# Performance work log

Hardware: AMD Instinct MI355X
Metric: run time of the kernel (lower is better)

The kernel has to match this reference:

```python
import jax, jax.numpy as jnp
import numpy as np

# state_composition -> (modality, length); slices are consecutive offsets into D_state
COMP = [("joint_pos", 64), ("joint_vel", 64), ("eef_pose", 32), ("force", 32)]
NUM_EMB = 32   # num_embodiments
HID = 512      # hidden_size
EMB = 1024     # embed_dim
B, T = 16, 32


def setup_inputs() -> dict:
    key = jax.random.key(0)
    ks = iter(jax.random.split(key, 64))
    D = sum(L for _, L in COMP)
    inp = {
        "state_btD": jax.random.normal(next(ks), (B, T, D), jnp.float32),
        "embodiment_id_bt1": jax.random.randint(next(ks), (B, T, 1), 0, NUM_EMB, dtype=jnp.int64),
    }
    for m, L in COMP:
        inp[f"W1_{m}"] = 0.02 * jax.random.normal(next(ks), (NUM_EMB, L, HID), jnp.float32)
        inp[f"b1_{m}"] = jnp.zeros((NUM_EMB, HID), jnp.float32)
        inp[f"W2_{m}"] = 0.02 * jax.random.normal(next(ks), (NUM_EMB, HID, EMB), jnp.float32)
        inp[f"b2_{m}"] = jnp.zeros((NUM_EMB, EMB), jnp.float32)
        inp[f"te_{m}"] = 0.02 * jax.random.normal(next(ks), (1, 1, EMB), jnp.float32)
    return inp


def _cat_mlp(x, cat, W1, b1, W2, b2):
    # x: (N, in_dim), cat: (N,) int ids. Mirrors CategorySpecificMLP:
    # per-token weight gather W[cat] then bmm (here einsum over the token axis).
    h = jax.nn.relu(jnp.einsum("ni,nih->nh", x, W1[cat]) + b1[cat])
    return jnp.einsum("nh,nhe->ne", h, W2[cat]) + b2[cat]


def reference(state_btD, embodiment_id_bt1,
              W1_joint_pos, b1_joint_pos, W2_joint_pos, b2_joint_pos, te_joint_pos,
              W1_joint_vel, b1_joint_vel, W2_joint_vel, b2_joint_vel, te_joint_vel,
              W1_eef_pose, b1_eef_pose, W2_eef_pose, b2_eef_pose, te_eef_pose,
              W1_force, b1_force, W2_force, b2_force, te_force):
    Bv, Tv, D = state_btD.shape
    # expand (B,1,1) -> (B,T,1) if needed, then flatten to per-token ids
    cat = jnp.broadcast_to(embodiment_id_bt1, (Bv, Tv, 1)).reshape(Bv * Tv)
    params = [
        (W1_joint_pos, b1_joint_pos, W2_joint_pos, b2_joint_pos, te_joint_pos),
        (W1_joint_vel, b1_joint_vel, W2_joint_vel, b2_joint_vel, te_joint_vel),
        (W1_eef_pose, b1_eef_pose, W2_eef_pose, b2_eef_pose, te_eef_pose),
        (W1_force, b1_force, W2_force, b2_force, te_force),
    ]
    toks = []
    off = 0
    for (m, L), (W1, b1, W2, b2, te) in zip(COMP, params):
        x = state_btD[..., off:off + L].reshape(Bv * Tv, L)
        off += L
        z = _cat_mlp(x, cat, W1, b1, W2, b2) + te.reshape(EMB)
        toks.append(z.reshape(Bv, Tv, 1, EMB))
    return jnp.concatenate(toks, axis=2)  # (B, T, M, embed_dim)
```

## Files before the change

### kernel.cpp

```cpp
#include <hip/hip_runtime.h>

#define NCAT 32
#define NTOK 512
#define HID  512
#define EMB  1024
#define DSTATE 192
#define CHUNK 32
#define MAXW 48


__global__ __launch_bounds__(512) void bucket_kernel(
    const int* __restrict__ ids, int* __restrict__ cnt, int* __restrict__ nW,
    int* __restrict__ work, int* __restrict__ toklist)
{
    __shared__ int scnt[NCAT];
    const int tid = threadIdx.x;
    if (tid < NCAT) scnt[tid] = 0;
    __syncthreads();
    const int c = ids[tid];
    const int pos = atomicAdd(&scnt[c], 1);
    toklist[c * NTOK + pos] = tid;
    __syncthreads();
    if (tid == 0) {
        int n1 = 0;
        for (int cc = 0; cc < NCAT; ++cc) {
            const int n = scnt[cc];
            cnt[cc] = n;
            for (int ch = 0; ch * CHUNK < n; ++ch) work[n1++] = cc | (ch << 8);
        }
        nW[0] = n1;
    }
}

__device__ __forceinline__ void async_copy16(void* lds_dst, const void* g_src) {
    __builtin_amdgcn_global_load_lds(
        (__attribute__((address_space(1))) void*)(g_src),
        (__attribute__((address_space(3))) void*)(lds_dst),
        16, 0, 0);
}

__global__ __launch_bounds__(256, 2) void layer1_kernel(
    const float* __restrict__ state,
    const int* __restrict__ cnt, const int* __restrict__ toklist,
    const int* __restrict__ nW, const int* __restrict__ work,
    const float* __restrict__ W1_0, const float* __restrict__ W1_1,
    const float* __restrict__ W1_2, const float* __restrict__ W1_3,
    const float* __restrict__ b1_0, const float* __restrict__ b1_1,
    const float* __restrict__ b1_2, const float* __restrict__ b1_3,
    float* __restrict__ H)
{
    const int slot = blockIdx.x, mod = blockIdx.y, z = blockIdx.z;
    if (slot >= nW[0]) return;
    const int ent = work[slot];
    const int cat = ent & 255, chunk = ent >> 8;
    const int nC = cnt[cat];
    const int start = chunk * CHUNK;
    int nThis = nC - start;
    if (nThis > CHUNK) nThis = CHUNK;
    const int tid = threadIdx.x;
    const int tg = tid >> 6;
    const int cg = tid & 63;

    const int L   = (mod < 2) ? 64 : 32;
    const int off = (mod == 0) ? 0 : (mod == 1) ? 64 : (mod == 2) ? 128 : 160;

    __shared__ float sX[64 * 32];
    __shared__ int sTok[CHUNK];
    if (tid < CHUNK) sTok[tid] = (tid < nThis) ? toklist[cat * NTOK + start + tid] : 0;
    __syncthreads();

    {
        const int tt = tid & 31, kg = tid >> 5;
        const int rpk = L >> 3;
        const float* src = state + (size_t)sTok[tt] * DSTATE + off + kg * rpk;
        const bool ok = tt < nThis;
        for (int j = 0; j < (rpk >> 2); ++j) {
            float4 v = make_float4(0.f, 0.f, 0.f, 0.f);
            if (ok) v = ((const float4*)src)[j];
            const int k0 = kg * rpk + (j << 2);
            sX[(k0 + 0) * 32 + tt] = v.x;
            sX[(k0 + 1) * 32 + tt] = v.y;
            sX[(k0 + 2) * 32 + tt] = v.z;
            sX[(k0 + 3) * 32 + tt] = v.w;
        }
    }
    __syncthreads();

    const float* W1 = (mod == 0) ? W1_0 : (mod == 1) ? W1_1 : (mod == 2) ? W1_2 : W1_3;
    const float* b1 = (mod == 0) ? b1_0 : (mod == 1) ? b1_1 : (mod == 2) ? b1_2 : b1_3;
    const int colA = z * 256 + (cg << 2);
    const float* Wc = W1 + (size_t)cat * L * HID + colA;
    const int hbase = tg << 3;
    const bool act = hbase < nThis;

    float4 acc[8];
#pragma unroll
    for (int i = 0; i < 8; ++i) acc[i] = make_float4(0.f, 0.f, 0.f, 0.f);

    if (act) {
#pragma unroll 4
        for (int k = 0; k < L; ++k) {
            const float4 w  = *(const float4*)(Wc + (size_t)k * HID);
            const float4 h0 = *(const float4*)(sX + k * 32 + hbase);
            const float4 h1 = *(const float4*)(sX + k * 32 + hbase + 4);
#define L1FMA(i, s) acc[i].x += (s)*w.x; acc[i].y += (s)*w.y; \
                    acc[i].z += (s)*w.z; acc[i].w += (s)*w.w;
            L1FMA(0, h0.x) L1FMA(1, h0.y) L1FMA(2, h0.z) L1FMA(3, h0.w)
            L1FMA(4, h1.x) L1FMA(5, h1.y) L1FMA(6, h1.z) L1FMA(7, h1.w)
#undef L1FMA
        }
    }

    const float4 b = *(const float4*)(b1 + cat * HID + colA);
#pragma unroll
    for (int i = 0; i < 8; ++i) {
        const int t = hbase + i;
        if (t >= nThis) break;
        float4 h;
        h.x = acc[i].x + b.x; h.x = h.x > 0.f ? h.x : 0.f;
        h.y = acc[i].y + b.y; h.y = h.y > 0.f ? h.y : 0.f;
        h.z = acc[i].z + b.z; h.z = h.z > 0.f ? h.z : 0.f;
        h.w = acc[i].w + b.w; h.w = h.w > 0.f ? h.w : 0.f;
        *(float4*)(H + (size_t)(sTok[t] * 4 + mod) * HID + colA) = h;
    }
}

__global__ __launch_bounds__(256, 1) void layer2_kernel(
    const int* __restrict__ cnt, const int* __restrict__ toklist,
    const int* __restrict__ nW, const int* __restrict__ work,
    const float* __restrict__ H,
    const float* __restrict__ W2_0, const float* __restrict__ W2_1,
    const float* __restrict__ W2_2, const float* __restrict__ W2_3,
    const float* __restrict__ b2_0, const float* __restrict__ b2_1,
    const float* __restrict__ b2_2, const float* __restrict__ b2_3,
    const float* __restrict__ te_0, const float* __restrict__ te_1,
    const float* __restrict__ te_2, const float* __restrict__ te_3,
    float* __restrict__ out)
{
    const int slot = blockIdx.x, mod = blockIdx.y, z = blockIdx.z;
    if (slot >= nW[0]) return;
    const int ent = work[slot];
    const int cat = ent & 255, chunk = ent >> 8;
    const int nC = cnt[cat];
    const int start = chunk * CHUNK;
    int nThis = nC - start;
    if (nThis > CHUNK) nThis = CHUNK;
    const int tid = threadIdx.x;
    const int tg = tid >> 6;
    const int cg = tid & 63;
    const int zbase = z * 512;

    __shared__ float sH[512 * 32];
    __shared__ float wbuf[2][8 * 512];
    __shared__ int sTok[CHUNK];

    if (tid < CHUNK) sTok[tid] = (tid < nThis) ? toklist[cat * NTOK + start + tid] : 0;
    __syncthreads();

    const float* W2 = (mod == 0) ? W2_0 : (mod == 1) ? W2_1 : (mod == 2) ? W2_2 : W2_3;
    const float* Wc = W2 + (size_t)cat * (HID * EMB) + zbase;

#define STAGE_TILE(T, wb) do {                                                  \
        const float* gsrc_ = Wc + (size_t)((T) * 8 + (tid >> 7)) * EMB          \
                             + ((tid & 127) << 2);                              \
        float* ldst_ = (wb) + ((tid >> 6) << 8);                                \
        async_copy16(ldst_,        gsrc_);                                      \
        async_copy16(ldst_ + 1024, gsrc_ + 2 * EMB);                            \
        async_copy16(ldst_ + 2048, gsrc_ + 4 * EMB);                            \
        async_copy16(ldst_ + 3072, gsrc_ + 6 * EMB);                            \
    } while (0)

    STAGE_TILE(0, wbuf[0]);

    {
        const int tt = tid & 31, kg = tid >> 5;
        const float* src = H + (size_t)(sTok[tt] * 4 + mod) * HID + (kg << 6);
        const bool ok = tt < nThis;
#pragma unroll
        for (int j = 0; j < 16; ++j) {
            float4 v = make_float4(0.f, 0.f, 0.f, 0.f);
            if (ok) v = ((const float4*)src)[j];
            const int k0 = (kg << 6) + (j << 2);
            sH[(k0 + 0) * 32 + tt] = v.x;
            sH[(k0 + 1) * 32 + tt] = v.y;
            sH[(k0 + 2) * 32 + tt] = v.z;
            sH[(k0 + 3) * 32 + tt] = v.w;
        }
    }
    __syncthreads();

    const int hbase = tg << 3;
    const int wcol  = cg << 2;
    const bool act  = hbase < nThis;

    float4 a0[8], a1[8];
#pragma unroll
    for (int i = 0; i < 8; ++i) {
        a0[i] = make_float4(0.f, 0.f, 0.f, 0.f);
        a1[i] = make_float4(0.f, 0.f, 0.f, 0.f);
    }

#pragma unroll 1
    for (int T = 0; T < 64; ++T) {
        if (T + 1 < 64) STAGE_TILE(T + 1, wbuf[(T + 1) & 1]);
        if (act) {
            const float* wb = wbuf[T & 1];
            const int kb = T << 3;
#pragma unroll
            for (int r = 0; r < 8; ++r) {
                const float4 h0 = *(const float4*)(sH + (kb + r) * 32 + hbase);
                const float4 h1 = *(const float4*)(sH + (kb + r) * 32 + hbase + 4);
                const float4 w0 = *(const float4*)(wb + r * 512 + wcol);
                const float4 w1 = *(const float4*)(wb + r * 512 + 256 + wcol);
#define FMA2(i, s) a0[i].x += (s)*w0.x; a0[i].y += (s)*w0.y;                    \
                   a0[i].z += (s)*w0.z; a0[i].w += (s)*w0.w;                    \
                   a1[i].x += (s)*w1.x; a1[i].y += (s)*w1.y;                    \
                   a1[i].z += (s)*w1.z; a1[i].w += (s)*w1.w;
                FMA2(0, h0.x) FMA2(1, h0.y) FMA2(2, h0.z) FMA2(3, h0.w)
                FMA2(4, h1.x) FMA2(5, h1.y) FMA2(6, h1.z) FMA2(7, h1.w)
#undef FMA2
            }
        }
        __syncthreads();
    }
#undef STAGE_TILE

    const float* b2 = (mod == 0) ? b2_0 : (mod == 1) ? b2_1 : (mod == 2) ? b2_2 : b2_3;
    const float* te = (mod == 0) ? te_0 : (mod == 1) ? te_1 : (mod == 2) ? te_2 : te_3;
    const int colA = zbase + wcol;
    const int colB = colA + 256;
    const float4 bA = *(const float4*)(b2 + cat * EMB + colA);
    const float4 bB = *(const float4*)(b2 + cat * EMB + colB);
    const float4 tA = *(const float4*)(te + colA);
    const float4 tB = *(const float4*)(te + colB);
#pragma unroll
    for (int i = 0; i < 8; ++i) {
        const int t = hbase + i;
        if (t >= nThis) break;
        float* op = out + (size_t)(sTok[t] * 4 + mod) * EMB;
        *(float4*)(op + colA) = make_float4(a0[i].x + bA.x + tA.x,
                                            a0[i].y + bA.y + tA.y,
                                            a0[i].z + bA.z + tA.z,
                                            a0[i].w + bA.w + tA.w);
        *(float4*)(op + colB) = make_float4(a1[i].x + bB.x + tB.x,
                                            a1[i].y + bB.y + tB.y,
                                            a1[i].z + bB.z + tB.z,
                                            a1[i].w + bB.w + tB.w);
    }
}

extern "C" void kernel_launch(void* const* d_in, const int* in_sizes, int n_in,
                              void* d_out, int out_size, void* d_ws, size_t ws_size,
                              hipStream_t stream) {
    const float* state = (const float*)d_in[0];
    const int*   ids   = (const int*)d_in[1];
    const float *W1[4], *b1[4], *W2[4], *b2[4], *te[4];
    for (int m = 0; m < 4; ++m) {
        W1[m] = (const float*)d_in[2 + 5 * m + 0];
        b1[m] = (const float*)d_in[2 + 5 * m + 1];
        W2[m] = (const float*)d_in[2 + 5 * m + 2];
        b2[m] = (const float*)d_in[2 + 5 * m + 3];
        te[m] = (const float*)d_in[2 + 5 * m + 4];
    }
    char* ws = (char*)d_ws;
    int*   cnt     = (int*)ws;
    int*   nW      = (int*)(ws + 128);
    int*   work    = (int*)(ws + 256);
    int*   toklist = (int*)(ws + 1024);
    float* H       = (float*)(ws + 66560);
    float* out     = (float*)d_out;

    bucket_kernel<<<1, 512, 0, stream>>>(ids, cnt, nW, work, toklist);
    layer1_kernel<<<dim3(MAXW, 4, 2), 256, 0, stream>>>(
        state, cnt, toklist, nW, work,
        W1[0], W1[1], W1[2], W1[3],
        b1[0], b1[1], b1[2], b1[3], H);
    layer2_kernel<<<dim3(MAXW, 4, 2), 256, 0, stream>>>(
        cnt, toklist, nW, work, H,
        W2[0], W2[1], W2[2], W2[3],
        b2[0], b2[1], b2[2], b2[3],
        te[0], te[1], te[2], te[3], out);
}
```

Before: 340.6 us.

## Fuse layer1 into layer2 kernel with swizzled LDS hidden tile and triple-buffered W2

Merges the two MLP layer kernels into one. Each block computes the full 512-wide hidden activation for its 32-token chunk straight into a swizzled shared-memory tile, so the global H round trip and one kernel launch go away. The W2 staging pipeline moves from double to triple buffering with explicit vmcnt waits and raw barriers to keep more loads in flight. In exchange, layer1 work is repeated across the two z-halves, and LDS use grows, which may limit occupancy.

```diff
diff --git a/kernel.cpp b/kernel.cpp
--- a/kernel.cpp
+++ b/kernel.cpp
@@ -39,7 +39,7 @@
         16, 0, 0);
 }
 
-__global__ __launch_bounds__(256, 2) void layer1_kernel(
+__global__ __launch_bounds__(256, 1) void fused_kernel(
     const float* __restrict__ state,
     const int* __restrict__ cnt, const int* __restrict__ toklist,
     const int* __restrict__ nW, const int* __restrict__ work,
@@ -47,88 +47,6 @@
     const float* __restrict__ W1_2, const float* __restrict__ W1_3,
     const float* __restrict__ b1_0, const float* __restrict__ b1_1,
     const float* __restrict__ b1_2, const float* __restrict__ b1_3,
-    float* __restrict__ H)
-{
-    const int slot = blockIdx.x, mod = blockIdx.y, z = blockIdx.z;
-    if (slot >= nW[0]) return;
-    const int ent = work[slot];
-    const int cat = ent & 255, chunk = ent >> 8;
-    const int nC = cnt[cat];
-    const int start = chunk * CHUNK;
-    int nThis = nC - start;
-    if (nThis > CHUNK) nThis = CHUNK;
-    const int tid = threadIdx.x;
-    const int tg = tid >> 6;
-    const int cg = tid & 63;
-
-    const int L   = (mod < 2) ? 64 : 32;
-    const int off = (mod == 0) ? 0 : (mod == 1) ? 64 : (mod == 2) ? 128 : 160;
-
-    __shared__ float sX[64 * 32];
-    __shared__ int sTok[CHUNK];
-    if (tid < CHUNK) sTok[tid] = (tid < nThis) ? toklist[cat * NTOK + start + tid] : 0;
-    __syncthreads();
-
-    {
-        const int tt = tid & 31, kg = tid >> 5;
-        const int rpk = L >> 3;
-        const float* src = state + (size_t)sTok[tt] * DSTATE + off + kg * rpk;
-        const bool ok = tt < nThis;
-        for (int j = 0; j < (rpk >> 2); ++j) {
-            float4 v = make_float4(0.f, 0.f, 0.f, 0.f);
-            if (ok) v = ((const float4*)src)[j];
-            const int k0 = kg * rpk + (j << 2);
-            sX[(k0 + 0) * 32 + tt] = v.x;
-            sX[(k0 + 1) * 32 + tt] = v.y;
-            sX[(k0 + 2) * 32 + tt] = v.z;
-            sX[(k0 + 3) * 32 + tt] = v.w;
-        }
-    }
-    __syncthreads();
-
-    const float* W1 = (mod == 0) ? W1_0 : (mod == 1) ? W1_1 : (mod == 2) ? W1_2 : W1_3;
-    const float* b1 = (mod == 0) ? b1_0 : (mod == 1) ? b1_1 : (mod == 2) ? b1_2 : b1_3;
-    const int colA = z * 256 + (cg << 2);
-    const float* Wc = W1 + (size_t)cat * L * HID + colA;
-    const int hbase = tg << 3;
-    const bool act = hbase < nThis;
-
-    float4 acc[8];
-#pragma unroll
-    for (int i = 0; i < 8; ++i) acc[i] = make_float4(0.f, 0.f, 0.f, 0.f);
-
-    if (act) {
-#pragma unroll 4
-        for (int k = 0; k < L; ++k) {
-            const float4 w  = *(const float4*)(Wc + (size_t)k * HID);
-            const float4 h0 = *(const float4*)(sX + k * 32 + hbase);
-            const float4 h1 = *(const float4*)(sX + k * 32 + hbase + 4);
-#define L1FMA(i, s) acc[i].x += (s)*w.x; acc[i].y += (s)*w.y; \
-                    acc[i].z += (s)*w.z; acc[i].w += (s)*w.w;
-            L1FMA(0, h0.x) L1FMA(1, h0.y) L1FMA(2, h0.z) L1FMA(3, h0.w)
-            L1FMA(4, h1.x) L1FMA(5, h1.y) L1FMA(6, h1.z) L1FMA(7, h1.w)
-#undef L1FMA
-        }
-    }
-
-    const float4 b = *(const float4*)(b1 + cat * HID + colA);
-#pragma unroll
-    for (int i = 0; i < 8; ++i) {
-        const int t = hbase + i;
-        if (t >= nThis) break;
-        float4 h;
-        h.x = acc[i].x + b.x; h.x = h.x > 0.f ? h.x : 0.f;
-        h.y = acc[i].y + b.y; h.y = h.y > 0.f ? h.y : 0.f;
-        h.z = acc[i].z + b.z; h.z = h.z > 0.f ? h.z : 0.f;
-        h.w = acc[i].w + b.w; h.w = h.w > 0.f ? h.w : 0.f;
-        *(float4*)(H + (size_t)(sTok[t] * 4 + mod) * HID + colA) = h;
-    }
-}
-
-__global__ __launch_bounds__(256, 1) void layer2_kernel(
-    const int* __restrict__ cnt, const int* __restrict__ toklist,
-    const int* __restrict__ nW, const int* __restrict__ work,
-    const float* __restrict__ H,
     const float* __restrict__ W2_0, const float* __restrict__ W2_1,
     const float* __restrict__ W2_2, const float* __restrict__ W2_3,
     const float* __restrict__ b2_0, const float* __restrict__ b2_1,
@@ -148,17 +66,79 @@
     const int tid = threadIdx.x;
     const int tg = tid >> 6;
     const int cg = tid & 63;
-    const int zbase = z * 512;
-
+
+    const int L   = (mod < 2) ? 64 : 32;
+    const int off = (mod == 0) ? 0 : (mod == 1) ? 64 : (mod == 2) ? 128 : 160;
+
+    __shared__ float sX[64 * 32];
     __shared__ float sH[512 * 32];
-    __shared__ float wbuf[2][8 * 512];
+    __shared__ float wbuf[3][8 * 512];
     __shared__ int sTok[CHUNK];
 
     if (tid < CHUNK) sTok[tid] = (tid < nThis) ? toklist[cat * NTOK + start + tid] : 0;
     __syncthreads();
 
+    {
+        const int tt = tid & 31, kg = tid >> 5;
+        const int rpk = L >> 3;
+        const float* src = state + (size_t)sTok[tt] * DSTATE + off + kg * rpk;
+        const bool ok = tt < nThis;
+        for (int j = 0; j < (rpk >> 2); ++j) {
+            float4 v = make_float4(0.f, 0.f, 0.f, 0.f);
+            if (ok) v = ((const float4*)src)[j];
+            const int k0 = kg * rpk + (j << 2);
+            sX[(k0 + 0) * 32 + tt] = v.x;
+            sX[(k0 + 1) * 32 + tt] = v.y;
+            sX[(k0 + 2) * 32 + tt] = v.z;
+            sX[(k0 + 3) * 32 + tt] = v.w;
+        }
+    }
+    __syncthreads();
+
+    const float* W1 = (mod == 0) ? W1_0 : (mod == 1) ? W1_1 : (mod == 2) ? W1_2 : W1_3;
+    const float* b1 = (mod == 0) ? b1_0 : (mod == 1) ? b1_1 : (mod == 2) ? b1_2 : b1_3;
+    const float* W1c = W1 + (size_t)cat * L * HID + 2 * tid;
+
+    float2 hacc[32];
+#pragma unroll
+    for (int t = 0; t < 32; ++t) hacc[t] = make_float2(0.f, 0.f);
+
+#pragma unroll 4
+    for (int k = 0; k < L; ++k) {
+        const float2 w = *(const float2*)(W1c + (size_t)k * HID);
+        const float4* xp = (const float4*)(sX + k * 32);
+#pragma unroll
+        for (int q = 0; q < 8; ++q) {
+            const float4 x4 = xp[q];
+            hacc[4*q+0].x += x4.x * w.x; hacc[4*q+0].y += x4.x * w.y;
+            hacc[4*q+1].x += x4.y * w.x; hacc[4*q+1].y += x4.y * w.y;
+            hacc[4*q+2].x += x4.z * w.x; hacc[4*q+2].y += x4.z * w.y;
+            hacc[4*q+3].x += x4.w * w.x; hacc[4*q+3].y += x4.w * w.y;
+        }
+    }
+    {
+        const float2 bb = *(const float2*)(b1 + cat * HID + 2 * tid);
+        float4* s4 = (float4*)sH;
+        const int key = tid & 7;
+        const int r0 = 2 * tid, r1 = 2 * tid + 1;
+#pragma unroll
+        for (int q = 0; q < 8; ++q) {
+            float4 v0, v1;
+            v0.x = fmaxf(hacc[4*q+0].x + bb.x, 0.f);
+            v0.y = fmaxf(hacc[4*q+1].x + bb.x, 0.f);
+            v0.z = fmaxf(hacc[4*q+2].x + bb.x, 0.f);
+            v0.w = fmaxf(hacc[4*q+3].x + bb.x, 0.f);
+            v1.x = fmaxf(hacc[4*q+0].y + bb.y, 0.f);
+            v1.y = fmaxf(hacc[4*q+1].y + bb.y, 0.f);
+            v1.z = fmaxf(hacc[4*q+2].y + bb.y, 0.f);
+            v1.w = fmaxf(hacc[4*q+3].y + bb.y, 0.f);
+            s4[r0 * 8 + (q ^ key)] = v0;
+            s4[r1 * 8 + (q ^ key)] = v1;
+        }
+    }
+
     const float* W2 = (mod == 0) ? W2_0 : (mod == 1) ? W2_1 : (mod == 2) ? W2_2 : W2_3;
-    const float* Wc = W2 + (size_t)cat * (HID * EMB) + zbase;
+    const float* Wc = W2 + (size_t)cat * (HID * EMB) + z * 512;
 
 #define STAGE_TILE(T, wb) do {                                                  \
         const float* gsrc_ = Wc + (size_t)((T) * 8 + (tid >> 7)) * EMB          \
@@ -171,25 +151,14 @@
     } while (0)
 
     STAGE_TILE(0, wbuf[0]);
-
-    {
-        const int tt = tid & 31, kg = tid >> 5;
-        const float* src = H + (size_t)(sTok[tt] * 4 + mod) * HID + (kg << 6);
-        const bool ok = tt < nThis;
-#pragma unroll
-        for (int j = 0; j < 16; ++j) {
-            float4 v = make_float4(0.f, 0.f, 0.f, 0.f);
-            if (ok) v = ((const float4*)src)[j];
-            const int k0 = (kg << 6) + (j << 2);
-            sH[(k0 + 0) * 32 + tt] = v.x;
-            sH[(k0 + 1) * 32 + tt] = v.y;
-            sH[(k0 + 2) * 32 + tt] = v.z;
-            sH[(k0 + 3) * 32 + tt] = v.w;
-        }
-    }
-    __syncthreads();
+    STAGE_TILE(1, wbuf[1]);
+    asm volatile("s_waitcnt vmcnt(4) lgkmcnt(0)" ::: "memory");
+    __builtin_amdgcn_s_barrier();
+    asm volatile("" ::: "memory");
+    __builtin_amdgcn_sched_barrier(0);
 
     const int hbase = tg << 3;
+    const int tq0   = tg << 1;
     const int wcol  = cg << 2;
     const bool act  = hbase < nThis;
 
@@ -200,16 +169,20 @@
         a1[i] = make_float4(0.f, 0.f, 0.f, 0.f);
     }
 
+    int bcur = 0;
 #pragma unroll 1
     for (int T = 0; T < 64; ++T) {
-        if (T + 1 < 64) STAGE_TILE(T + 1, wbuf[(T + 1) & 1]);
+        int b2i = bcur + 2; if (b2i >= 3) b2i -= 3;
+        if (T + 2 < 64) STAGE_TILE(T + 2, wbuf[b2i]);
         if (act) {
-            const float* wb = wbuf[T & 1];
+            const float* wb = wbuf[bcur];
             const int kb = T << 3;
 #pragma unroll
             for (int r = 0; r < 8; ++r) {
-                const float4 h0 = *(const float4*)(sH + (kb + r) * 32 + hbase);
-                const float4 h1 = *(const float4*)(sH + (kb + r) * 32 + hbase + 4);
+                const int k  = kb + r;
+                const int kk = (k >> 1) & 7;
+                const float4 h0 = ((const float4*)sH)[k * 8 + (tq0 ^ kk)];
+                const float4 h1 = ((const float4*)sH)[k * 8 + ((tq0 + 1) ^ kk)];
                 const float4 w0 = *(const float4*)(wb + r * 512 + wcol);
                 const float4 w1 = *(const float4*)(wb + r * 512 + 256 + wcol);
 #define FMA2(i, s) a0[i].x += (s)*w0.x; a0[i].y += (s)*w0.y;                    \
@@ -221,13 +194,20 @@
 #undef FMA2
             }
         }
-        __syncthreads();
+        if (T < 63) {
+            if (T + 2 < 64) { asm volatile("s_waitcnt vmcnt(4)" ::: "memory"); }
+            else            { asm volatile("s_waitcnt vmcnt(0)" ::: "memory"); }
+            __builtin_amdgcn_s_barrier();
+            asm volatile("" ::: "memory");
+            __builtin_amdgcn_sched_barrier(0);
+        }
+        bcur = bcur + 1; if (bcur == 3) bcur = 0;
     }
 #undef STAGE_TILE
 
     const float* b2 = (mod == 0) ? b2_0 : (mod == 1) ? b2_1 : (mod == 2) ? b2_2 : b2_3;
     const float* te = (mod == 0) ? te_0 : (mod == 1) ? te_1 : (mod == 2) ? te_2 : te_3;
-    const int colA = zbase + wcol;
+    const int colA = z * 512 + wcol;
     const int colB = colA + 256;
     const float4 bA = *(const float4*)(b2 + cat * EMB + colA);
     const float4 bB = *(const float4*)(b2 + cat * EMB + colB);
@@ -267,16 +247,13 @@
     int*   nW      = (int*)(ws + 128);
     int*   work    = (int*)(ws + 256);
     int*   toklist = (int*)(ws + 1024);
-    float* H       = (float*)(ws + 66560);
     float* out     = (float*)d_out;
 
     bucket_kernel<<<1, 512, 0, stream>>>(ids, cnt, nW, work, toklist);
-    layer1_kernel<<<dim3(MAXW, 4, 2), 256, 0, stream>>>(
+    fused_kernel<<<dim3(MAXW, 4, 2), 256, 0, stream>>>(
         state, cnt, toklist, nW, work,
         W1[0], W1[1], W1[2], W1[3],
-        b1[0], b1[1], b1[2], b1[3], H);
-    layer2_kernel<<<dim3(MAXW, 4, 2), 256, 0, stream>>>(
-        cnt, toklist, nW, work, H,
+        b1[0], b1[1], b1[2], b1[3],
         W2[0], W2[1], W2[2], W2[3],
         b2[0], b2[1], b2[2], b2[3],
         te[0], te[1], te[2], te[3], out);
```

Measured after the change: 328.6 us. -3.5%, faster.
